# Optimization experiments

Hardware: AMD Instinct MI355X
Metric: run time of the kernel (lower is better)

## Reference

```python
import jax, jax.numpy as jnp
import numpy as np

K = 16  # neighbors

def knn_idx(a, b, k):
    # a:(B,3,N1), b:(B,3,N2) -> idx (B,N1,k) of nearest neighbors (max of neg sq dist)
    inner = jnp.einsum('bcn,bcm->bnm', a, b)              # (B,N1,N2)
    a2 = jnp.sum(a * a, axis=1)                           # (B,N1)
    b2 = jnp.sum(b * b, axis=1)                           # (B,N2)
    neg_d = 2.0 * inner - a2[:, :, None] - b2[:, None, :]
    _, idx = jax.lax.top_k(neg_d, k)                      # (B,N1,k)
    return idx

def group_points(fea, idx):
    # fea:(B,C,M), idx:(B,N,k) -> (B,C,N,k)
    return jax.vmap(lambda f, i: f[:, i])(fea, idx)

def setup_inputs() -> dict:
    key = jax.random.key(0)
    ks = jax.random.split(key, 8)
    B, N, C, OUT = 4, 8192, 64, 64
    return {
        'xyz':   jax.random.normal(ks[0], (B, 3, N), jnp.float32),
        'xyz_s': jax.random.normal(ks[1], (B, 3, N), jnp.float32),
        'fea':   jax.random.normal(ks[2], (B, C, N), jnp.float32),
        'fea_s': jax.random.normal(ks[3], (B, C, N), jnp.float32),
        'Wg': jax.random.normal(ks[4], (OUT, 10), jnp.float32) * 0.3,
        'bg': jax.random.normal(ks[5], (OUT,), jnp.float32) * 0.1,
        'Wf': jax.random.normal(ks[6], (OUT, 2 * C), jnp.float32) * 0.1,
        'bf': jax.random.normal(ks[7], (OUT,), jnp.float32) * 0.1,
    }

def reference(xyz, xyz_s, fea, fea_s, Wg, bg, Wf, bf):
    idx = knn_idx(xyz, xyz_s, K)                          # (B,N,k)

    # --- geometric edge features (B,10,N,k) ---
    xyz_knn = group_points(xyz_s, idx)                    # (B,3,N,k)
    xyz_c = jnp.broadcast_to(xyz[:, :, :, None], xyz_knn.shape)
    xyz_r = xyz_c - xyz_knn
    xyz_d = jnp.sqrt(jnp.sum(xyz_r * xyz_r, axis=1, keepdims=True))
    geo = jnp.concatenate([xyz_d, xyz_c, xyz_knn, xyz_r], axis=1)  # (B,10,N,k)

    # --- feature edge features (B,2C,N,k) ---
    fea_knn = group_points(fea_s, idx)                    # (B,C,N,k)
    fea_c = jnp.broadcast_to(fea[:, :, :, None], fea_knn.shape)
    edge = jnp.concatenate([fea_c, fea_knn], axis=1)      # (B,2C,N,k)

    # 1x1 conv + bias + ReLU for both branches
    g = jax.nn.relu(jnp.einsum('oc,bcnk->bonk', Wg, geo) + bg[None, :, None, None])
    f = jax.nn.relu(jnp.einsum('oc,bcnk->bonk', Wf, edge) + bf[None, :, None, None])

    # elementwise modulation + max over neighbors
    return jnp.max(g * f, axis=-1)                        # (B,OUT,N)
```

## Files before the change

kernel.cpp:

```cpp
#include <hip/hip_runtime.h>
#include <math.h>

#define NPTS 8192
#define NB   4
#define KNN  16
#define NC   64
#define NQ   (NB * NPTS)
#define ECAP 20
#define ILCAP 66

__global__ __launch_bounds__(64) void prep_kernel(
    const float* __restrict__ xyz, const float* __restrict__ xyz_s,
    const float* __restrict__ fea, const float* __restrict__ fea_s,
    const float* __restrict__ Wg,  const float* __restrict__ bg,
    const float* __restrict__ Wf,  const float* __restrict__ bf,
    float4* __restrict__ cand, float2* __restrict__ GF, float2* __restrict__ CF)
{
    __shared__ float wt[64 * 64];
    __shared__ float gw[3 * 64];
    __shared__ float bias2[2 * 64];
    int tid   = threadIdx.x;
    int phase = blockIdx.x & 1;
    int g     = (blockIdx.x >> 1) * 64 + tid;
    int b     = g >> 13, m = g & (NPTS - 1);

    for (int i = tid; i < 4096; i += 64) {
        int o = i >> 6, c = i & 63;
        wt[c * 64 + o] = Wf[o * 128 + (phase ? c : 64 + c)];
    }
    for (int i = tid; i < 192; i += 64) {
        int d = i >> 6, o = i & 63;
        gw[d * 64 + o] = phase ? (Wg[o * 10 + 1 + d] + Wg[o * 10 + 7 + d])
                               : (Wg[o * 10 + 4 + d] - Wg[o * 10 + 7 + d]);
    }
    {
        bias2[tid]      = phase ? bg[tid] : 0.f;
        bias2[64 + tid] = phase ? bf[tid] : 0.f;
    }
    __syncthreads();

    const float* P = phase ? xyz : xyz_s;
    const float* F = phase ? fea : fea_s;
    float x = P[(b * 3 + 0) * NPTS + m];
    float y = P[(b * 3 + 1) * NPTS + m];
    float z = P[(b * 3 + 2) * NPTS + m];
    if (!phase) cand[b * NPTS + m] = make_float4(x, y, z, x * x + y * y + z * z);

    float acc[NC];
    #pragma unroll
    for (int o = 0; o < NC; o++) acc[o] = 0.f;
    for (int c = 0; c < NC; c++) {
        float v = F[(size_t)(b * NC + c) * NPTS + m];
        const float4* w4 = (const float4*)&wt[c * 64];
        #pragma unroll
        for (int o4 = 0; o4 < 16; o4++) {
            float4 w = w4[o4];
            acc[o4*4+0] = fmaf(w.x, v, acc[o4*4+0]);
            acc[o4*4+1] = fmaf(w.y, v, acc[o4*4+1]);
            acc[o4*4+2] = fmaf(w.z, v, acc[o4*4+2]);
            acc[o4*4+3] = fmaf(w.w, v, acc[o4*4+3]);
        }
    }
    float2* O = (phase ? CF : GF) + ((size_t)(b * NPTS + m)) * NC;
    #pragma unroll
    for (int o = 0; o < NC; o++) {
        float geo = fmaf(gw[o], x, fmaf(gw[64 + o], y, gw[128 + o] * z));
        O[o] = make_float2(geo + bias2[o], acc[o] + bias2[64 + o]);
    }
}

__global__ __launch_bounds__(512, 4) void knn_fused4(
    const float4* __restrict__ cand, const float* __restrict__ xyz,
    int* __restrict__ idxout)
{
    __shared__ float4 qt_lds[64];
    __shared__ float  mxs[64][ILCAP];
    __shared__ unsigned int  el[8][64][ECAP];
    __shared__ unsigned char ecnt[8][64];

    int tid = threadIdx.x;
    int lane = tid & 63, w = tid >> 6;
    int bid = blockIdx.x;
    int b = bid >> 7;
    int qb = (bid & 127) * 64;

    if (tid < 64) {
        int q = qb + tid;
        float x = xyz[(b * 3 + 0) * NPTS + q];
        float y = xyz[(b * 3 + 1) * NPTS + q];
        float z = xyz[(b * 3 + 2) * NPTS + q];
        qt_lds[tid] = make_float4(2.f * x, 2.f * y, 2.f * z, 0.f);
    }

    const float4* cb = cand + b * NPTS;
    int cbase = (w << 10) + lane;
    float4 c[16];
    #pragma unroll
    for (int s = 0; s < 16; s++) c[s] = cb[cbase + (s << 6)];
    #pragma unroll
    for (int s = 0; s < 16; s++)
        asm volatile("" : "+v"(c[s].x), "+v"(c[s].y), "+v"(c[s].z), "+v"(c[s].w));
    __syncthreads();

    for (int qi = 0; qi < 64; ++qi) {
        float4 qt = qt_lds[qi];
        float M0 = -3.0e38f, M1 = -3.0e38f;
        #pragma unroll
        for (int s = 0; s < 16; s += 2) {
            float sc0 = fmaf(c[s].x, qt.x, fmaf(c[s].y, qt.y,
                        fmaf(c[s].z, qt.z, -c[s].w)));
            float sc1 = fmaf(c[s+1].x, qt.x, fmaf(c[s+1].y, qt.y,
                        fmaf(c[s+1].z, qt.z, -c[s+1].w)));
            M0 = fmaxf(M0, sc0);
            M1 = fmaxf(M1, sc1);
        }
        float gmx = fmaxf(M0, M1);
        gmx = fmaxf(gmx, __shfl_xor(gmx, 1));
        gmx = fmaxf(gmx, __shfl_xor(gmx, 2));
        gmx = fmaxf(gmx, __shfl_xor(gmx, 4));
        if ((lane & 7) == 0) mxs[qi][(w << 3) + (lane >> 3)] = gmx;
    }
    __syncthreads();

    for (int qq = w * 8; qq < w * 8 + 8; ++qq) {
        float v = mxs[qq][lane];
        #pragma unroll
        for (int k = 2; k <= 64; k <<= 1) {
            #pragma unroll
            for (int j = k >> 1; j > 0; j >>= 1) {
                float o = __shfl_xor(v, j);
                bool up = ((lane & k) == 0);
                bool lower = ((lane & j) == 0);
                v = (up == lower) ? fminf(v, o) : fmaxf(v, o);
            }
        }
        float t = __shfl(v, 48);
        if (lane == 0) qt_lds[qq].w = t;
    }
    __syncthreads();

    unsigned long long lmask = (1ull << lane) - 1ull;
    for (int qi = 0; qi < 64; ++qi) {
        float4 qt = qt_lds[qi];
        unsigned msk = 0;
        #pragma unroll
        for (int s = 0; s < 16; s++) {
            float sc = fmaf(c[s].x, qt.x, fmaf(c[s].y, qt.y,
                       fmaf(c[s].z, qt.z, -c[s].w)));
            msk |= (sc >= qt.w) ? (1u << s) : 0u;
        }
        unsigned long long m = __ballot(msk != 0u);
        if (msk) {
            unsigned pos = (unsigned)__popcll(m & lmask);
            if (pos < ECAP)
                el[w][qi][pos] = ((unsigned)lane << 16) | msk;
        }
        if (lane == 0) {
            unsigned tot = (unsigned)__popcll(m);
            ecnt[w][qi] = (unsigned char)(tot < ECAP ? tot : ECAP);
        }
    }
    __syncthreads();

    if (tid < 64) {
        int qi = tid;
        unsigned* il = (unsigned*)&mxs[qi][0];
        int cnt = 0;
        for (int w2 = 0; w2 < 8; w2++) {
            int cn = ecnt[w2][qi];
            for (int j = 0; j < cn; j++) {
                unsigned e = el[w2][qi][j];
                int base = (w2 << 10) + (int)(e >> 16);
                unsigned mk = e & 0xFFFFu;
                while (mk) {
                    int s = __builtin_ctz(mk);
                    mk &= mk - 1u;
                    if (cnt < ILCAP) il[cnt++] = (unsigned)(base + (s << 6));
                }
            }
        }

        float4 qt = qt_lds[qi];
        unsigned long long s16[KNN];
        #pragma unroll
        for (int j = 0; j < KNN; j++) s16[j] = 0ull;

        for (int j0 = 0; j0 < cnt; j0 += 4) {
            int li[4];
            float4 cd[4];
            #pragma unroll
            for (int t = 0; t < 4; t++) {
                int j = j0 + t;
                li[t] = (j < cnt) ? (int)il[j] : -1;
            }
            #pragma unroll
            for (int t = 0; t < 4; t++)
                if (li[t] >= 0) cd[t] = cb[li[t]];
            #pragma unroll
            for (int t = 0; t < 4; t++) {
                if (li[t] < 0) continue;
                float sc = fmaf(cd[t].x, qt.x, fmaf(cd[t].y, qt.y,
                           fmaf(cd[t].z, qt.z, -cd[t].w)));
                unsigned u = __float_as_uint(sc);
                u ^= (unsigned)((int)u >> 31) | 0x80000000u;
                unsigned long long key =
                    ((unsigned long long)u << 32) | (unsigned)(8191 - li[t]);
                if (key > s16[0]) {
                    bool cj = true;
                    #pragma unroll
                    for (int t2 = 0; t2 < KNN; t2++) {
                        bool cn2 = (t2 < KNN - 1) ? (key > s16[t2 + 1]) : false;
                        unsigned long long fv = cj ? key : s16[t2];
                        s16[t2] = cn2 ? s16[t2 + 1] : fv;
                        cj = cn2;
                    }
                }
            }
        }
        int* op = idxout + (((size_t)(b * NPTS + qb + qi)) << 4);
        #pragma unroll
        for (int j = 0; j < KNN; j++)
            op[j] = 8191 - (int)(s16[j] & 0xFFFFFFFFull);
    }
}

__global__ __launch_bounds__(256) void fuse_kernel(
    const float* __restrict__ xyz, const float* __restrict__ Wg,
    const float4* __restrict__ cand, const float2* __restrict__ GF,
    const float2* __restrict__ CF, const int* __restrict__ idxb,
    float* __restrict__ out)
{
    __shared__ float tile[16 * 65];
    int tid = threadIdx.x;
    int o = tid & 63, w = tid >> 6;
    int b = blockIdx.x >> 9;
    int nt = (blockIdx.x & 511) << 4;
    float wd = Wg[o * 10];

    const float4* cb = cand + b * NPTS;
    const float2* gb = GF + (size_t)b * NPTS * NC;

    for (int i = 0; i < 4; i++) {
        int q = nt + w * 4 + i;
        size_t qb = (size_t)(b * NPTS + q);
        float qx = xyz[(b * 3 + 0) * NPTS + q];
        float qy = xyz[(b * 3 + 1) * NPTS + q];
        float qz = xyz[(b * 3 + 2) * NPTS + q];
        float2 cf = CF[qb * NC + o];
        const int* ip = idxb + qb * KNN;

        int mi[16];
        #pragma unroll
        for (int kk = 0; kk < 16; kk++) mi[kk] = ip[kk];

        float r = 0.f;
        #pragma unroll
        for (int h = 0; h < 2; h++) {
            float4 cd[8];
            float2 gf[8];
            #pragma unroll
            for (int t = 0; t < 8; t++) cd[t] = cb[mi[h * 8 + t]];
            #pragma unroll
            for (int t = 0; t < 8; t++)
                gf[t] = gb[(size_t)mi[h * 8 + t] * NC + o];
            #pragma unroll
            for (int t = 0; t < 8; t++) {
                float dx = qx - cd[t].x, dy = qy - cd[t].y, dz = qz - cd[t].z;
                float d = sqrtf(fmaf(dx, dx, fmaf(dy, dy, dz * dz)));
                float gpre = cf.x + fmaf(wd, d, gf[t].x);
                float fpre = cf.y + gf[t].y;
                r = fmaxf(r, fmaxf(gpre, 0.f) * fmaxf(fpre, 0.f));
            }
        }
        tile[(w * 4 + i) * 65 + o] = r;
    }
    __syncthreads();
    int row = tid >> 2, cg = (tid & 3) * 4;
    float* orow = out + (size_t)(b * NC + row) * NPTS + nt + cg;
    #pragma unroll
    for (int j = 0; j < 4; j++) orow[j] = tile[(cg + j) * 65 + row];
}

extern "C" void kernel_launch(void* const* d_in, const int* in_sizes, int n_in,
                              void* d_out, int out_size, void* d_ws, size_t ws_size,
                              hipStream_t stream) {
    const float* xyz   = (const float*)d_in[0];
    const float* xyz_s = (const float*)d_in[1];
    const float* fea   = (const float*)d_in[2];
    const float* fea_s = (const float*)d_in[3];
    const float* Wg    = (const float*)d_in[4];
    const float* bg    = (const float*)d_in[5];
    const float* Wf    = (const float*)d_in[6];
    const float* bf    = (const float*)d_in[7];
    float* out = (float*)d_out;

    char* ws = (char*)d_ws;
    float4* cand = (float4*)ws;                 ws += (size_t)NQ * 16;
    float2* GF   = (float2*)ws;                 ws += (size_t)NQ * NC * 8;
    float2* CF   = (float2*)ws;                 ws += (size_t)NQ * NC * 8;
    int*    idxb = (int*)ws;

    prep_kernel<<<(NQ / 64) * 2, 64, 0, stream>>>(
        xyz, xyz_s, fea, fea_s, Wg, bg, Wf, bf, cand, GF, CF);
    knn_fused4<<<NQ / 64, 512, 0, stream>>>(cand, xyz, idxb);
    fuse_kernel<<<NB * (NPTS / 16), 256, 0, stream>>>(
        xyz, Wg, cand, GF, CF, idxb, out);
}
```

Before: 181.7 us.

## Remap prep kernel threads to output channels with coalesced output stores

The prep kernel now assigns each thread to one output channel and loops over 64 points, instead of one thread per point looping over channels. Weights are read straight from global memory into registers, so the shared-memory transpose and its barrier go away. The float2 output stores become coalesced across the wavefront. In exchange, feature rows are read with wavefront-uniform float4 broadcast loads and xyz is reloaded per point, which puts more load traffic through the cache.

```diff
diff --git a/kernel.cpp b/kernel.cpp
--- a/kernel.cpp
+++ b/kernel.cpp
@@ -16,56 +16,56 @@
     const float* __restrict__ Wf,  const float* __restrict__ bf,
     float4* __restrict__ cand, float2* __restrict__ GF, float2* __restrict__ CF)
 {
-    __shared__ float wt[64 * 64];
-    __shared__ float gw[3 * 64];
-    __shared__ float bias2[2 * 64];
-    int tid   = threadIdx.x;
+    int o     = threadIdx.x;
     int phase = blockIdx.x & 1;
-    int g     = (blockIdx.x >> 1) * 64 + tid;
-    int b     = g >> 13, m = g & (NPTS - 1);
-
-    for (int i = tid; i < 4096; i += 64) {
-        int o = i >> 6, c = i & 63;
-        wt[c * 64 + o] = Wf[o * 128 + (phase ? c : 64 + c)];
-    }
-    for (int i = tid; i < 192; i += 64) {
-        int d = i >> 6, o = i & 63;
-        gw[d * 64 + o] = phase ? (Wg[o * 10 + 1 + d] + Wg[o * 10 + 7 + d])
-                               : (Wg[o * 10 + 4 + d] - Wg[o * 10 + 7 + d]);
-    }
-    {
-        bias2[tid]      = phase ? bg[tid] : 0.f;
-        bias2[64 + tid] = phase ? bf[tid] : 0.f;
-    }
-    __syncthreads();
+    int g     = (blockIdx.x >> 1) * 64;
+    int b     = g >> 13, p0 = g & (NPTS - 1);
 
     const float* P = phase ? xyz : xyz_s;
     const float* F = phase ? fea : fea_s;
-    float x = P[(b * 3 + 0) * NPTS + m];
-    float y = P[(b * 3 + 1) * NPTS + m];
-    float z = P[(b * 3 + 2) * NPTS + m];
-    if (!phase) cand[b * NPTS + m] = make_float4(x, y, z, x * x + y * y + z * z);
-
-    float acc[NC];
+
+    if (!phase) {
+        float x = xyz_s[(b * 3 + 0) * NPTS + p0 + o];
+        float y = xyz_s[(b * 3 + 1) * NPTS + p0 + o];
+        float z = xyz_s[(b * 3 + 2) * NPTS + p0 + o];
+        cand[b * NPTS + p0 + o] = make_float4(x, y, z, x * x + y * y + z * z);
+    }
+
+    const float* wrow = Wf + o * 128 + (phase ? 0 : 64);
+    float gwx = phase ? (Wg[o * 10 + 1] + Wg[o * 10 + 7])
+                      : (Wg[o * 10 + 4] - Wg[o * 10 + 7]);
+    float gwy = phase ? (Wg[o * 10 + 2] + Wg[o * 10 + 8])
+                      : (Wg[o * 10 + 5] - Wg[o * 10 + 8]);
+    float gwz = phase ? (Wg[o * 10 + 3] + Wg[o * 10 + 9])
+                      : (Wg[o * 10 + 6] - Wg[o * 10 + 9]);
+    float bgo = phase ? bg[o] : 0.f;
+    float bfo = phase ? bf[o] : 0.f;
+
+    float acc[64];
     #pragma unroll
-    for (int o = 0; o < NC; o++) acc[o] = 0.f;
-    for (int c = 0; c < NC; c++) {
-        float v = F[(size_t)(b * NC + c) * NPTS + m];
-        const float4* w4 = (const float4*)&wt[c * 64];
-        #pragma unroll
-        for (int o4 = 0; o4 < 16; o4++) {
-            float4 w = w4[o4];
-            acc[o4*4+0] = fmaf(w.x, v, acc[o4*4+0]);
-            acc[o4*4+1] = fmaf(w.y, v, acc[o4*4+1]);
-            acc[o4*4+2] = fmaf(w.z, v, acc[o4*4+2]);
-            acc[o4*4+3] = fmaf(w.w, v, acc[o4*4+3]);
-        }
-    }
-    float2* O = (phase ? CF : GF) + ((size_t)(b * NPTS + m)) * NC;
-    #pragma unroll
-    for (int o = 0; o < NC; o++) {
-        float geo = fmaf(gw[o], x, fmaf(gw[64 + o], y, gw[128 + o] * z));
-        O[o] = make_float2(geo + bias2[o], acc[o] + bias2[64 + o]);
+    for (int p = 0; p < 64; p++) acc[p] = 0.f;
+
+    for (int c = 0; c < 64; c++) {
+        float wv = wrow[c];
+        const float4* fr =
+            (const float4*)(F + (size_t)(b * NC + c) * NPTS + p0);
+        #pragma unroll
+        for (int p4 = 0; p4 < 16; p4++) {
+            float4 v = fr[p4];
+            acc[p4 * 4 + 0] = fmaf(wv, v.x, acc[p4 * 4 + 0]);
+            acc[p4 * 4 + 1] = fmaf(wv, v.y, acc[p4 * 4 + 1]);
+            acc[p4 * 4 + 2] = fmaf(wv, v.z, acc[p4 * 4 + 2]);
+            acc[p4 * 4 + 3] = fmaf(wv, v.w, acc[p4 * 4 + 3]);
+        }
+    }
+
+    float2* O = (phase ? CF : GF) + ((size_t)(b * NPTS + p0)) * NC + o;
+    for (int p = 0; p < 64; p++) {
+        float x = P[(b * 3 + 0) * NPTS + p0 + p];
+        float y = P[(b * 3 + 1) * NPTS + p0 + p];
+        float z = P[(b * 3 + 2) * NPTS + p0 + p];
+        float geo = fmaf(gwx, x, fmaf(gwy, y, gwz * z)) + bgo;
+        O[(size_t)p * NC] = make_float2(geo, acc[p] + bfo);
     }
 }
 
```

Result: no change. 178.9 us (median of 2 runs) (-1.5%).
